# Kernel tuning notes

Measured on AMD Instinct MI355X. Metric: run time of the kernel, lower is better.

## Reference

```python
import jax, jax.numpy as jnp
import numpy as np

T, B, N, C, H, D = 4, 8, 1024, 512, 8, 64
EPS = 1e-5


def setup_inputs() -> dict:
    key = jax.random.key(0)
    ks = jax.random.split(key, 16)
    d = {"x": jax.random.normal(ks[0], (T, B, N, C), jnp.float32)}
    for i, nm in enumerate(["q", "k", "v", "p"]):
        kW, kmu, kvar = jax.random.split(ks[1 + i], 3)
        d[f"W{nm}"] = jax.random.normal(kW, (C, C), jnp.float32) * 0.02
        d[f"b{nm}"] = jnp.zeros((C,), jnp.float32)
        d[f"g{nm}"] = jnp.ones((C,), jnp.float32)
        d[f"beta{nm}"] = jnp.zeros((C,), jnp.float32)
        d[f"mu{nm}"] = jax.random.normal(kmu, (C,), jnp.float32) * 0.1
        d[f"var{nm}"] = jax.random.uniform(kvar, (C,), jnp.float32, 0.5, 1.5)
    return d


def _lin_bn(z, W, b, g, beta, mu, var):
    # nn.Linear over channel dim, then eval-mode BatchNorm1d per channel
    y = jnp.einsum('tbnc,dc->tbnd', z, W) + b
    return (y - mu) * (g * jax.lax.rsqrt(var + EPS)) + beta


def _to_heads(z):
    # (t,b,n,c) -> (t,b,h,n,d)
    return z.reshape(T, B, N, H, D).transpose(0, 1, 3, 2, 4)


def reference(x, Wq, bq, gq, betaq, muq, varq,
              Wk, bk, gk, betak, muk, vark,
              Wv, bv, gv, betav, muv, varv,
              Wp, bp, gp, betap, mup, varp):
    q = _to_heads(_lin_bn(x, Wq, bq, gq, betaq, muq, varq))
    k = _to_heads(_lin_bn(x, Wk, bk, gk, betak, muk, vark))
    v = _to_heads(_lin_bn(x, Wv, bv, gv, betav, muv, varv))
    # attention_linear variant: kv = (k^T @ v) / N ; y = q @ kv
    kv = jnp.einsum('tbhnd,tbhne->tbhde', k, v) / float(N)  # (t,b,h,d,d)
    y = jnp.einsum('tbhnd,tbhde->tbhne', q, kv)             # (t,b,h,n,d)
    y = y.transpose(0, 1, 3, 2, 4).reshape(T, B, N, C)
    return _lin_bn(y, Wp, bp, gp, betap, mup, varp)
```

## Files before the change

kernel.cpp:

```cpp
#include <hip/hip_runtime.h>

#define T_ 4
#define B_ 8
#define N_ 1024
#define C_ 512
#define H_ 8
#define D_ 64
#define M_ (T_*B_*N_)
#define TB_ (T_*B_)

typedef __bf16 bf16;
typedef __bf16 bf16x4 __attribute__((ext_vector_type(4)));
typedef __bf16 bf16x8 __attribute__((ext_vector_type(8)));
typedef float f32x4 __attribute__((ext_vector_type(4)));

__device__ __forceinline__ void gload16(const void* g, void* l) {
  __builtin_amdgcn_global_load_lds(
      (const __attribute__((address_space(1))) void*)g,
      (__attribute__((address_space(3))) void*)l, 16, 0, 0);
}

struct PtrPack { const float* p[24]; };

__global__ __launch_bounds__(256)
void prep_all(PtrPack pk, bf16* __restrict__ WB, float* __restrict__ BS) {
  const int mat = blockIdx.x >> 9, d = blockIdx.x & 511;
  const float* W    = pk.p[6*mat + 0];
  const float* b    = pk.p[6*mat + 1];
  const float* g    = pk.p[6*mat + 2];
  const float* beta = pk.p[6*mat + 3];
  const float* mu   = pk.p[6*mat + 4];
  const float* var  = pk.p[6*mat + 5];
  float s = g[d] * rsqrtf(var[d] + 1e-5f);
  if (threadIdx.x == 0) BS[mat*512 + d] = (b[d] - mu[d]) * s + beta[d];
  bf16* Wout = WB + (size_t)mat * 262144 + (size_t)d * 512;
  for (int c = threadIdx.x; c < 512; c += 256)
    Wout[c] = (bf16)(W[(size_t)d * 512 + c] * s);
}

__global__ __launch_bounds__(256)
void prep_wqT(const float* __restrict__ W, const float* __restrict__ g,
              const float* __restrict__ var, bf16* __restrict__ WqT) {
  const int di = blockIdx.x >> 3, ci = blockIdx.x & 7;
  const int t = threadIdx.x;
  __shared__ float lds[64][65];
  const int rgrp = t >> 4, k = t & 15;
#pragma unroll
  for (int p = 0; p < 4; p++) {
    int r = p * 16 + rgrp;
    int d = di * 64 + r;
    float s = g[d] * rsqrtf(var[d] + 1e-5f);
    float4 v = *(const float4*)(W + (size_t)d * 512 + ci * 64 + k * 4);
    lds[r][k*4+0] = v.x * s; lds[r][k*4+1] = v.y * s;
    lds[r][k*4+2] = v.z * s; lds[r][k*4+3] = v.w * s;
  }
  __syncthreads();
#pragma unroll
  for (int p = 0; p < 16; p++) {
    int c = p * 4 + (t >> 6), dd = t & 63;
    WqT[(size_t)(ci*64 + c) * 512 + di*64 + dd] = (bf16)lds[dd][c];
  }
}

__global__ __launch_bounds__(256)
void cvt_x_t(const float* __restrict__ x, bf16* __restrict__ xb,
             bf16* __restrict__ xT, float* __restrict__ spart) {
  const int bid = blockIdx.x;
  const int tb = bid >> 7, nc = (bid >> 3) & 15, cc = bid & 7;
  const int t = threadIdx.x;
  __shared__ float lds[64][65];
  __shared__ float sred[16][64];
  const float* xbase = x + (size_t)tb * 524288 + (size_t)nc * 64 * 512 + cc * 64;
  bf16* xbb = xb + (size_t)tb * 524288 + (size_t)nc * 64 * 512 + cc * 64;
  bf16* xTb = xT + (size_t)tb * 524288 + (size_t)(cc * 64) * 1024 + nc * 64;
  const int rgrp = t >> 4, k = t & 15;
  float s0 = 0, s1 = 0, s2 = 0, s3 = 0;
#pragma unroll
  for (int p = 0; p < 4; p++) {
    int r = p * 16 + rgrp;
    float4 v = *(const float4*)(xbase + (size_t)r * 512 + k * 4);
    bf16x4 o; o[0]=(bf16)v.x; o[1]=(bf16)v.y; o[2]=(bf16)v.z; o[3]=(bf16)v.w;
    *(bf16x4*)(xbb + (size_t)r * 512 + k * 4) = o;
    lds[r][k*4+0]=v.x; lds[r][k*4+1]=v.y; lds[r][k*4+2]=v.z; lds[r][k*4+3]=v.w;
    s0 += v.x; s1 += v.y; s2 += v.z; s3 += v.w;
  }
  sred[rgrp][k*4+0]=s0; sred[rgrp][k*4+1]=s1; sred[rgrp][k*4+2]=s2; sred[rgrp][k*4+3]=s3;
  __syncthreads();
#pragma unroll
  for (int p = 0; p < 16; p++) {
    int c = p * 4 + (t >> 6), n = t & 63;
    xTb[(size_t)c * 1024 + n] = (bf16)lds[n][c];
  }
  if (t < 64) {
    float tot = 0;
#pragma unroll
    for (int rg = 0; rg < 16; rg++) tot += sred[rg][t];
    spart[(size_t)((tb*8 + cc)*16 + nc) * 64 + t] = tot;
  }
}

__global__ __launch_bounds__(512)
void s_fin(const float* __restrict__ spart, float* __restrict__ sv) {
  const int tb = blockIdx.x, c = threadIdx.x;
  const int cc = c >> 6, cl = c & 63;
  float tot = 0;
#pragma unroll
  for (int ncf = 0; ncf < 16; ncf++)
    tot += spart[(size_t)((tb*8 + cc)*16 + ncf) * 64 + cl];
  sv[tb * 512 + c] = tot;
}

__global__ __launch_bounds__(512)
void ksvs(const bf16* __restrict__ WB, const float* __restrict__ sv,
          float* __restrict__ ksv) {
  const int tb = blockIdx.x, m = blockIdx.y;
  __shared__ float sl[512];
  sl[threadIdx.x] = sv[tb * 512 + threadIdx.x];
  __syncthreads();
  const bf16* Wrow = WB + (size_t)(m + 1) * 262144 + (size_t)threadIdx.x * 512;
  float acc = 0;
  for (int c = 0; c < 512; c += 8) {
    bf16x8 wv = *(const bf16x8*)(Wrow + c);
#pragma unroll
    for (int i = 0; i < 8; i++) acc += (float)wv[i] * sl[c + i];
  }
  ksv[m * 16384 + tb * 512 + threadIdx.x] = acc;
}

template <int NKT, int MT, int NT, bool BF16OUT, bool HASBIAS>
__global__ __launch_bounds__(256)
void gemm_b(const bf16* __restrict__ Abase, size_t Astr,
            const bf16* __restrict__ Btbase, size_t Btstr,
            const float* __restrict__ biasb, int biasstr,
            bf16* __restrict__ ob, float* __restrict__ of, size_t Ostr) {
  constexpr int K = NKT * 64;
  constexpr int PERB = MT * NT;
  const int bid = blockIdx.x;
  const int xcd = bid & 7, j9 = bid >> 3;
  const int bat = xcd + 8 * (j9 / PERB);
  const int tile = j9 % PERB;
  const int mi = tile / NT, ni = tile % NT;
  const bf16* A = Abase + (size_t)bat * Astr;
  const bf16* Bt = Btbase + (size_t)bat * Btstr;
  const int m0 = mi * 128, n0 = ni * 128;
  __shared__ __align__(16) bf16 As[128][64];
  __shared__ __align__(16) bf16 Bs[128][64];
  const int tid = threadIdx.x, w = tid >> 6, l = tid & 63;
  const int wm = w >> 1, wn = w & 1;
  const int lr = l & 15, lq = l >> 4, l7 = l & 7, lh = l >> 3;
  const int srcc = (l7 ^ lh) * 8;
  f32x4 acc[4][4] = {};
  for (int kt = 0; kt < NKT; kt++) {
#pragma unroll
    for (int i = 0; i < 4; i++) {
      int rb = w * 32 + i * 8;
      gload16(A  + (size_t)(m0 + rb + lh) * K + kt * 64 + srcc, &As[rb][0]);
      gload16(Bt + (size_t)(n0 + rb + lh) * K + kt * 64 + srcc, &Bs[rb][0]);
    }
    __syncthreads();
    bf16x8 af[4][2], bv[4][2];
#pragma unroll
    for (int f = 0; f < 4; f++) {
      int ra = wm * 64 + f * 16 + lr, rb2 = wn * 64 + f * 16 + lr;
#pragma unroll
      for (int s = 0; s < 2; s++) {
        af[f][s] = *(const bf16x8*)&As[ra][((s*4+lq) ^ (ra & 7)) * 8];
        bv[f][s] = *(const bf16x8*)&Bs[rb2][((s*4+lq) ^ (rb2 & 7)) * 8];
      }
    }
#pragma unroll
    for (int mt = 0; mt < 4; mt++)
#pragma unroll
      for (int nt = 0; nt < 4; nt++)
#pragma unroll
        for (int s = 0; s < 2; s++)
          acc[mt][nt] = __builtin_amdgcn_mfma_f32_16x16x32_bf16(
              af[mt][s], bv[nt][s], acc[mt][nt], 0, 0, 0);
    __syncthreads();
  }
  const int ldo = NT * 128;
#pragma unroll
  for (int mt = 0; mt < 4; mt++)
#pragma unroll
    for (int nt = 0; nt < 4; nt++) {
      int j = n0 + wn * 64 + nt * 16 + lr;
      float bj = HASBIAS ? biasb[(size_t)bat * biasstr + j] : 0.f;
      size_t mrow = (size_t)m0 + wm * 64 + mt * 16 + lq * 4;
#pragma unroll
      for (int r = 0; r < 4; r++) {
        if constexpr (BF16OUT)
          ob[(size_t)bat * Ostr + (mrow + r) * ldo + j] = (bf16)(acc[mt][nt][r] + bj);
        else
          of[(size_t)bat * Ostr + (mrow + r) * ldo + j] = acc[mt][nt][r] + bj;
      }
    }
}

__global__ __launch_bounds__(256)
void kvz(const bf16* __restrict__ KGb, const bf16* __restrict__ WB,
         const float* __restrict__ BS, const float* __restrict__ ksv,
         bf16* __restrict__ ZT, float* __restrict__ cpart) {
  const int gid = blockIdx.x, tb = gid >> 3, h = gid & 7;
  const int t = threadIdx.x, w = t >> 6, l = t & 63;
  const int lr = l & 15, lq = l >> 4;
  __shared__ __align__(16) char lds[65536 + 65536 + 8192];
  bf16* bufA = (bf16*)lds;
  bf16* bufV = (bf16*)(lds + 65536);
  bf16* kvb  = (bf16*)(lds + 131072);

#pragma unroll
  for (int i = 0; i < 16; i++) {
    int r = i * 4 + w;
    gload16(KGb + (size_t)tb * 262144 + (size_t)(64*h + r) * 512 + ((l ^ (r & 7)) * 8),
            bufA + r * 512);
    gload16(WB + 2u * 262144 + (size_t)(64*h + r) * 512 + ((l ^ (r & 7)) * 8),
            bufV + r * 512);
  }
  __syncthreads();

  f32x4 acc2[4][4] = {};
#pragma unroll
  for (int ks = 0; ks < 4; ks++) {
    int gch = w * 16 + ks * 4 + lq;
    bf16x8 af2[4], bv2[4];
#pragma unroll
    for (int mf = 0; mf < 4; mf++) {
      int d = mf * 16 + lr;
      af2[mf] = *(const bf16x8*)&bufA[d * 512 + ((gch ^ (d & 7)) * 8)];
    }
#pragma unroll
    for (int nf = 0; nf < 4; nf++) {
      int e = nf * 16 + lr;
      bv2[nf] = *(const bf16x8*)&bufV[e * 512 + ((gch ^ (e & 7)) * 8)];
    }
#pragma unroll
    for (int mf = 0; mf < 4; mf++)
#pragma unroll
      for (int nf = 0; nf < 4; nf++)
        acc2[mf][nf] = __builtin_amdgcn_mfma_f32_16x16x32_bf16(
            af2[mf], bv2[nf], acc2[mf][nf], 0, 0, 0);
  }
  __syncthreads();

  float* part = (float*)lds + w * 4096;
#pragma unroll
  for (int mf = 0; mf < 4; mf++)
#pragma unroll
    for (int nf = 0; nf < 4; nf++)
#pragma unroll
      for (int r = 0; r < 4; r++) {
        int d = mf * 16 + lq * 4 + r, e = nf * 16 + lr;
        part[d * 64 + e] = acc2[mf][nf][r];
      }
  __syncthreads();
  {
    const float inv = 1.f / 1024.f;
    const float* pb = (const float*)lds;
#pragma unroll
    for (int jj = 0; jj < 16; jj++) {
      int flat = jj * 256 + t, d = flat >> 6, e = flat & 63;
      float s = pb[flat] + pb[4096 + flat] + pb[8192 + flat] + pb[12288 + flat];
      float ksh = ksv[tb * 512 + 64*h + d];
      float vsh = ksv[16384 + tb * 512 + 64*h + e];
      float bkh = BS[512 + 64*h + d];
      float bvh = BS[1024 + 64*h + e];
      float kv = (s + ksh * bvh + bkh * vsh) * inv + bkh * bvh;
      kvb[d * 64 + (((e >> 3) ^ (d & 7)) * 8 + (e & 7))] = (bf16)kv;
    }
  }
  __syncthreads();

#pragma unroll
  for (int i = 0; i < 16; i++) {
    int rb = i * 32 + w * 8;
    int r = rb + (l >> 3);
    gload16(WB + 3u * 262144 + (size_t)r * 512 + 64*h + (((l & 7) ^ (r & 7)) * 8),
            bufA + rb * 64);
  }
  __syncthreads();

  f32x4 acc3[4][8] = {};
#pragma unroll
  for (int s = 0; s < 2; s++) {
    bf16x8 af3[4];
#pragma unroll
    for (int mf = 0; mf < 4; mf++) {
      int d = mf * 16 + lr;
      af3[mf] = *(const bf16x8*)&kvb[d * 64 + (((s*4+lq) ^ (d & 7)) * 8)];
    }
#pragma unroll
    for (int nf = 0; nf < 8; nf++) {
      int jj = w * 128 + nf * 16 + lr;
      bf16x8 b3 = *(const bf16x8*)&bufA[jj * 64 + (((s*4+lq) ^ (jj & 7)) * 8)];
#pragma unroll
      for (int mf = 0; mf < 4; mf++)
        acc3[mf][nf] = __builtin_amdgcn_mfma_f32_16x16x32_bf16(
            af3[mf], b3, acc3[mf][nf], 0, 0, 0);
    }
  }

  bf16* zbase = ZT + (size_t)tb * 262144 + 64*h;
#pragma unroll
  for (int nf = 0; nf < 8; nf++) {
    int jj = w * 128 + nf * 16 + lr;
    float cp = 0.f;
#pragma unroll
    for (int mf = 0; mf < 4; mf++) {
      bf16x4 o;
#pragma unroll
      for (int r = 0; r < 4; r++) {
        o[r] = (bf16)acc3[mf][nf][r];
        cp += acc3[mf][nf][r] * BS[64*h + mf*16 + lq*4 + r];
      }
      *(bf16x4*)(zbase + (size_t)jj * 512 + mf * 16 + lq * 4) = o;
    }
    cp += __shfl_xor(cp, 16);
    cp += __shfl_xor(cp, 32);
    if (lq == 0) cpart[(size_t)(tb * 8 + h) * 512 + jj] = cp;
  }
}

__global__ __launch_bounds__(512)
void cvfin(const float* __restrict__ cpart, const float* __restrict__ BS,
           float* __restrict__ cvec) {
  const int tb = blockIdx.x, j = threadIdx.x;
  float s = BS[1536 + j];
#pragma unroll
  for (int h = 0; h < 8; h++) s += cpart[(size_t)(tb * 8 + h) * 512 + j];
  cvec[tb * 512 + j] = s;
}

extern "C" void kernel_launch(void* const* d_in, const int* in_sizes, int n_in,
                              void* d_out, int out_size, void* d_ws, size_t ws_size,
                              hipStream_t stream) {
  const float* x = (const float*)d_in[0];
  char* ws = (char*)d_ws;
  bf16*  xb    = (bf16*)(ws + 0);
  bf16*  xT    = (bf16*)(ws + 33554432);
  bf16*  Gb    = (bf16*)(ws + 67108864);
  bf16*  KGb   = (bf16*)(ws + 83886080);
  bf16*  ZT    = (bf16*)(ws + 100663296);
  bf16*  VT    = (bf16*)(ws + 117440512);
  bf16*  WB    = (bf16*)(ws + 134217728);
  bf16*  WqT   = (bf16*)(ws + 136314880);
  float* BS    = (float*)(ws + 136839168);
  float* sv    = (float*)(ws + 136847360);
  float* ksv   = (float*)(ws + 136912896);
  float* cvec  = (float*)(ws + 137041920);
  float* cpart = (float*)(ws + 137107456);
  float* spart = (float*)(ws + 137631744);
  (void)in_sizes; (void)n_in; (void)out_size; (void)ws_size;

  PtrPack pk;
  for (int i = 0; i < 24; i++) pk.p[i] = (const float*)d_in[1 + i];

  prep_all<<<2048, 256, 0, stream>>>(pk, WB, BS);
  prep_wqT<<<64, 256, 0, stream>>>((const float*)d_in[1], (const float*)d_in[3],
                                   (const float*)d_in[6], WqT);
  cvt_x_t<<<4096, 256, 0, stream>>>(x, xb, xT, spart);
  s_fin<<<32, 512, 0, stream>>>(spart, sv);
  ksvs<<<dim3(32, 2), 512, 0, stream>>>(WB, sv, ksv);
  gemm_b<16, 4, 4, true, false><<<512, 256, 0, stream>>>(
      xT, 524288, xT, 524288, nullptr, 0, Gb, nullptr, 262144);
  gemm_b<8, 4, 4, true, false><<<512, 256, 0, stream>>>(
      WB + 262144, 0, Gb, 262144, nullptr, 0, KGb, nullptr, 262144);
  kvz<<<256, 256, 0, stream>>>(KGb, WB, BS, ksv, ZT, cpart);
  cvfin<<<32, 512, 0, stream>>>(cpart, BS, cvec);
  gemm_b<8, 4, 4, true, false><<<512, 256, 0, stream>>>(
      ZT, 262144, WqT, 0, nullptr, 0, VT, nullptr, 262144);
  gemm_b<8, 8, 4, false, true><<<1024, 256, 0, stream>>>(
      xb, 524288, VT, 262144, cvec, 512, nullptr, (float*)d_out, 524288);
}
```

Baseline: 147.7 us.

## Exploit Gram symmetry, double-buffer GEMM tiles, and fuse small reduction kernels

The x^T x Gram GEMM now computes only the upper-triangular 128x128 tiles (10 of 16 per batch) and writes each off-diagonal tile's transpose through LDS. The GEMM mainloop gains double-buffered LDS staging so the next k-tile loads overlap the MFMAs on the current one. The s_fin and cvfin reduction kernels are folded into ksvs and the final GEMM's bias epilogue, removing two launches. The costs are double the LDS per block and a redundant per-element cpart sum in the epilogue; a leftover dead loop remains in the transpose path.

```diff
diff --git a/kernel.cpp b/kernel.cpp
--- a/kernel.cpp
+++ b/kernel.cpp
@@ -100,72 +100,78 @@
 }
 
 __global__ __launch_bounds__(512)
-void s_fin(const float* __restrict__ spart, float* __restrict__ sv) {
-  const int tb = blockIdx.x, c = threadIdx.x;
-  const int cc = c >> 6, cl = c & 63;
+void ksvs(const bf16* __restrict__ WB, const float* __restrict__ spart,
+          float* __restrict__ ksv) {
+  const int tb = blockIdx.x, m = blockIdx.y;
+  const int c = threadIdx.x, cc = c >> 6, cl = c & 63;
+  __shared__ float sl[512];
   float tot = 0;
 #pragma unroll
   for (int ncf = 0; ncf < 16; ncf++)
     tot += spart[(size_t)((tb*8 + cc)*16 + ncf) * 64 + cl];
-  sv[tb * 512 + c] = tot;
-}
-
-__global__ __launch_bounds__(512)
-void ksvs(const bf16* __restrict__ WB, const float* __restrict__ sv,
-          float* __restrict__ ksv) {
-  const int tb = blockIdx.x, m = blockIdx.y;
-  __shared__ float sl[512];
-  sl[threadIdx.x] = sv[tb * 512 + threadIdx.x];
-  __syncthreads();
-  const bf16* Wrow = WB + (size_t)(m + 1) * 262144 + (size_t)threadIdx.x * 512;
+  sl[c] = tot;
+  __syncthreads();
+  const bf16* Wrow = WB + (size_t)(m + 1) * 262144 + (size_t)c * 512;
   float acc = 0;
-  for (int c = 0; c < 512; c += 8) {
-    bf16x8 wv = *(const bf16x8*)(Wrow + c);
-#pragma unroll
-    for (int i = 0; i < 8; i++) acc += (float)wv[i] * sl[c + i];
-  }
-  ksv[m * 16384 + tb * 512 + threadIdx.x] = acc;
-}
-
-template <int NKT, int MT, int NT, bool BF16OUT, bool HASBIAS>
+  for (int k = 0; k < 512; k += 8) {
+    bf16x8 wv = *(const bf16x8*)(Wrow + k);
+#pragma unroll
+    for (int i = 0; i < 8; i++) acc += (float)wv[i] * sl[k + i];
+  }
+  ksv[m * 16384 + tb * 512 + c] = acc;
+}
+
+template <int NKT, int MT, int NT, bool BF16OUT, bool BIAS2, bool SYM>
 __global__ __launch_bounds__(256)
-void gemm_b(const bf16* __restrict__ Abase, size_t Astr,
-            const bf16* __restrict__ Btbase, size_t Btstr,
-            const float* __restrict__ biasb, int biasstr,
-            bf16* __restrict__ ob, float* __restrict__ of, size_t Ostr) {
+void gemm2(const bf16* __restrict__ Abase, size_t Astr,
+           const bf16* __restrict__ Btbase, size_t Btstr,
+           const float* __restrict__ BSb, const float* __restrict__ cpart,
+           bf16* __restrict__ ob, float* __restrict__ of, size_t Ostr) {
   constexpr int K = NKT * 64;
-  constexpr int PERB = MT * NT;
+  constexpr int PERB = SYM ? (MT * (MT + 1) / 2) : (MT * NT);
   const int bid = blockIdx.x;
   const int xcd = bid & 7, j9 = bid >> 3;
   const int bat = xcd + 8 * (j9 / PERB);
   const int tile = j9 % PERB;
-  const int mi = tile / NT, ni = tile % NT;
+  int mi, ni;
+  if constexpr (SYM) {
+    if (tile < 4)      { mi = 0; ni = tile; }
+    else if (tile < 7) { mi = 1; ni = tile - 3; }
+    else if (tile < 9) { mi = 2; ni = tile - 5; }
+    else               { mi = 3; ni = 3; }
+  } else { mi = tile / NT; ni = tile % NT; }
   const bf16* A = Abase + (size_t)bat * Astr;
   const bf16* Bt = Btbase + (size_t)bat * Btstr;
   const int m0 = mi * 128, n0 = ni * 128;
-  __shared__ __align__(16) bf16 As[128][64];
-  __shared__ __align__(16) bf16 Bs[128][64];
+  __shared__ __align__(16) bf16 As[2][128][64];
+  __shared__ __align__(16) bf16 Bs[2][128][64];
   const int tid = threadIdx.x, w = tid >> 6, l = tid & 63;
   const int wm = w >> 1, wn = w & 1;
   const int lr = l & 15, lq = l >> 4, l7 = l & 7, lh = l >> 3;
   const int srcc = (l7 ^ lh) * 8;
   f32x4 acc[4][4] = {};
+
+#define STG2(buf, kt)                                                         \
+  { _Pragma("unroll") for (int i_ = 0; i_ < 4; i_++) {                        \
+      int rb_ = w * 32 + i_ * 8;                                              \
+      gload16(A  + (size_t)(m0 + rb_ + lh) * K + (kt) * 64 + srcc,            \
+              &As[buf][rb_][0]);                                              \
+      gload16(Bt + (size_t)(n0 + rb_ + lh) * K + (kt) * 64 + srcc,            \
+              &Bs[buf][rb_][0]); } }
+
+  STG2(0, 0);
+  __syncthreads();
   for (int kt = 0; kt < NKT; kt++) {
-#pragma unroll
-    for (int i = 0; i < 4; i++) {
-      int rb = w * 32 + i * 8;
-      gload16(A  + (size_t)(m0 + rb + lh) * K + kt * 64 + srcc, &As[rb][0]);
-      gload16(Bt + (size_t)(n0 + rb + lh) * K + kt * 64 + srcc, &Bs[rb][0]);
-    }
-    __syncthreads();
+    const int cur = kt & 1;
+    if (kt + 1 < NKT) STG2(cur ^ 1, kt + 1);
     bf16x8 af[4][2], bv[4][2];
 #pragma unroll
     for (int f = 0; f < 4; f++) {
       int ra = wm * 64 + f * 16 + lr, rb2 = wn * 64 + f * 16 + lr;
 #pragma unroll
       for (int s = 0; s < 2; s++) {
-        af[f][s] = *(const bf16x8*)&As[ra][((s*4+lq) ^ (ra & 7)) * 8];
-        bv[f][s] = *(const bf16x8*)&Bs[rb2][((s*4+lq) ^ (rb2 & 7)) * 8];
+        af[f][s] = *(const bf16x8*)&As[cur][ra][((s*4+lq) ^ (ra & 7)) * 8];
+        bv[f][s] = *(const bf16x8*)&Bs[cur][rb2][((s*4+lq) ^ (rb2 & 7)) * 8];
       }
     }
 #pragma unroll
@@ -178,13 +184,21 @@
               af[mt][s], bv[nt][s], acc[mt][nt], 0, 0, 0);
     __syncthreads();
   }
+#undef STG2
+
   const int ldo = NT * 128;
 #pragma unroll
   for (int mt = 0; mt < 4; mt++)
 #pragma unroll
     for (int nt = 0; nt < 4; nt++) {
       int j = n0 + wn * 64 + nt * 16 + lr;
-      float bj = HASBIAS ? biasb[(size_t)bat * biasstr + j] : 0.f;
+      float bj = 0.f;
+      if constexpr (BIAS2) {
+        bj = BSb[1536 + j];
+#pragma unroll
+        for (int h = 0; h < 8; h++)
+          bj += cpart[(size_t)(bat * 8 + h) * 512 + j];
+      }
       size_t mrow = (size_t)m0 + wm * 64 + mt * 16 + lq * 4;
 #pragma unroll
       for (int r = 0; r < 4; r++) {
@@ -194,6 +208,40 @@
           of[(size_t)bat * Ostr + (mrow + r) * ldo + j] = acc[mt][nt][r] + bj;
       }
     }
+
+  if constexpr (SYM) {
+    if (mi != ni) {
+      bf16* TB = (bf16*)As;
+      __syncthreads();
+#pragma unroll
+      for (int mt = 0; mt < 4; mt++)
+#pragma unroll
+        for (int nt = 0; nt < 4; nt++) {
+          int a = wn * 64 + nt * 16 + lr;
+#pragma unroll
+          for (int r = 0; r < 4; r++) {
+            int b = wm * 64 + mt * 16 + lq * 4 + r;
+            TB[(a * 128 + b) ^ ((a & 7) << 3)] = (bf16)acc[mt][nt][r];
+          }
+        }
+      __syncthreads();
+      const int a = tid >> 1, half = tid & 1;
+#pragma unroll
+      for (int i = 0; i < 4; i++) {
+        int a2 = a + (i >> 1) * 64;
+        int c8 = half * 8 + (i & 1) * 4;
+        (void)a2; (void)c8;
+      }
+#pragma unroll
+      for (int i = 0; i < 8; i++) {
+        int rowa = tid >> 1;
+        int c8 = half * 8 + i;
+        bf16x8 v = *(const bf16x8*)&TB[(rowa * 128 + c8 * 8) ^ ((rowa & 7) << 3)];
+        *(bf16x8*)(ob + (size_t)bat * Ostr + (size_t)(ni * 128 + rowa) * ldo +
+                   mi * 128 + c8 * 8) = v;
+      }
+    }
+  }
 }
 
 __global__ __launch_bounds__(256)
@@ -318,16 +366,6 @@
     cp += __shfl_xor(cp, 32);
     if (lq == 0) cpart[(size_t)(tb * 8 + h) * 512 + jj] = cp;
   }
-}
-
-__global__ __launch_bounds__(512)
-void cvfin(const float* __restrict__ cpart, const float* __restrict__ BS,
-           float* __restrict__ cvec) {
-  const int tb = blockIdx.x, j = threadIdx.x;
-  float s = BS[1536 + j];
-#pragma unroll
-  for (int h = 0; h < 8; h++) s += cpart[(size_t)(tb * 8 + h) * 512 + j];
-  cvec[tb * 512 + j] = s;
 }
 
 extern "C" void kernel_launch(void* const* d_in, const int* in_sizes, int n_in,
@@ -344,11 +382,9 @@
   bf16*  WB    = (bf16*)(ws + 134217728);
   bf16*  WqT   = (bf16*)(ws + 136314880);
   float* BS    = (float*)(ws + 136839168);
-  float* sv    = (float*)(ws + 136847360);
-  float* ksv   = (float*)(ws + 136912896);
-  float* cvec  = (float*)(ws + 137041920);
-  float* cpart = (float*)(ws + 137107456);
-  float* spart = (float*)(ws + 137631744);
+  float* ksv   = (float*)(ws + 136847360);
+  float* cpart = (float*)(ws + 136978432);
+  float* spart = (float*)(ws + 137502720);
   (void)in_sizes; (void)n_in; (void)out_size; (void)ws_size;
 
   PtrPack pk;
@@ -358,16 +394,14 @@
   prep_wqT<<<64, 256, 0, stream>>>((const float*)d_in[1], (const float*)d_in[3],
                                    (const float*)d_in[6], WqT);
   cvt_x_t<<<4096, 256, 0, stream>>>(x, xb, xT, spart);
-  s_fin<<<32, 512, 0, stream>>>(spart, sv);
-  ksvs<<<dim3(32, 2), 512, 0, stream>>>(WB, sv, ksv);
-  gemm_b<16, 4, 4, true, false><<<512, 256, 0, stream>>>(
-      xT, 524288, xT, 524288, nullptr, 0, Gb, nullptr, 262144);
-  gemm_b<8, 4, 4, true, false><<<512, 256, 0, stream>>>(
-      WB + 262144, 0, Gb, 262144, nullptr, 0, KGb, nullptr, 262144);
+  ksvs<<<dim3(32, 2), 512, 0, stream>>>(WB, spart, ksv);
+  gemm2<16, 4, 4, true, false, true><<<320, 256, 0, stream>>>(
+      xT, 524288, xT, 524288, nullptr, nullptr, Gb, nullptr, 262144);
+  gemm2<8, 4, 4, true, false, false><<<512, 256, 0, stream>>>(
+      WB + 262144, 0, Gb, 262144, nullptr, nullptr, KGb, nullptr, 262144);
   kvz<<<256, 256, 0, stream>>>(KGb, WB, BS, ksv, ZT, cpart);
-  cvfin<<<32, 512, 0, stream>>>(cpart, BS, cvec);
-  gemm_b<8, 4, 4, true, false><<<512, 256, 0, stream>>>(
-      ZT, 262144, WqT, 0, nullptr, 0, VT, nullptr, 262144);
-  gemm_b<8, 8, 4, false, true><<<1024, 256, 0, stream>>>(
-      xb, 524288, VT, 262144, cvec, 512, nullptr, (float*)d_out, 524288);
-}
+  gemm2<8, 4, 4, true, false, false><<<512, 256, 0, stream>>>(
+      ZT, 262144, WqT, 0, nullptr, nullptr, VT, nullptr, 262144);
+  gemm2<8, 8, 4, false, true, false><<<1024, 256, 0, stream>>>(
+      xb, 524288, VT, 262144, BS, cpart, nullptr, (float*)d_out, 524288);
+}
```

Result: no change. 149.7 us (+1.4%).
